# Kernel optimization log

Measured on AMD Instinct MI355X. Metric: run time of the kernel, lower is better.

The kernel has to match this reference:

```python
import jax, jax.numpy as jnp
import numpy as np

B, H, W, C, NH, WS = 8, 113, 113, 512, 8, 7


def setup_inputs() -> dict:
    key = jax.random.key(0)
    k1, k2, k3 = jax.random.split(key, 3)
    x = jax.random.normal(k1, (B, H * W, C), jnp.float32)
    # torch Linear(embed_dims, 3*embed_dims, bias=False); stored as [C, 3C] for x @ W
    w_qkv = jax.random.normal(k2, (C, 3 * C), jnp.float32) * 0.02
    w_proj = jax.random.normal(k3, (C, C), jnp.float32) * 0.02
    b_proj = jnp.zeros((C,), jnp.float32)
    return {"x": x, "w_qkv": w_qkv, "w_proj": w_proj, "b_proj": b_proj, "h": H, "w": W}


def reference(x, w_qkv, w_proj, b_proj, h, w):
    b, n, c = x.shape
    ws, nh = WS, NH
    hd = c // nh
    scale = hd ** -0.5
    pad_b = (ws - h % ws) % ws
    pad_r = (ws - w % ws) % ws
    xi = x.reshape(b, h, w, c)
    xi = jnp.pad(xi, ((0, 0), (0, pad_b), (0, pad_r), (0, 0)))
    Hp, Wp = h + pad_b, w + pad_r
    _h, _w = Hp // ws, Wp // ws
    N = ws * ws
    nw = _h * _w

    # padding mask: 1 on padded rows/cols (matches torch fill of last pad_b rows / pad_r cols;
    # when pad==0 torch fills everything with 1 but mask differences are identically 0 either way)
    rows = jnp.arange(Hp)
    cols = jnp.arange(Wp)
    mask = ((rows[:, None] >= Hp - pad_b) | (cols[None, :] >= Wp - pad_r)).astype(x.dtype)
    mask = mask.reshape(_h, ws, _w, ws).transpose(0, 2, 1, 3).reshape(nw, N)
    am = mask[:, None, :] - mask[:, :, None]  # (nw, N, N)
    am = jnp.where(am != 0, jnp.asarray(-1000.0, x.dtype), jnp.asarray(0.0, x.dtype))

    # window partition: (b, _h, _w, ws, ws, c) -> (b, nw, N, c)
    xw = xi.reshape(b, _h, ws, _w, ws, c).transpose(0, 1, 3, 2, 4, 5).reshape(b, nw, N, c)

    qkv = (xw @ w_qkv).reshape(b, nw, N, 3, nh, hd)
    qkv = jnp.moveaxis(qkv, 3, 0)  # (3, b, nw, N, nh, hd)
    q = qkv[0].transpose(0, 1, 3, 2, 4)  # (b, nw, nh, N, hd)
    k = qkv[1].transpose(0, 1, 3, 2, 4)
    v = qkv[2].transpose(0, 1, 3, 2, 4)

    attn = jnp.einsum('bwhnd,bwhmd->bwhnm', q, k) * scale
    attn = attn + am[None, :, None, :, :]
    attn = jax.nn.softmax(attn, axis=-1)
    out = jnp.einsum('bwhnm,bwhmd->bwhnd', attn, v)  # (b, nw, nh, N, hd)

    # window merge back to (b, Hp, Wp, c)
    out = out.transpose(0, 1, 3, 2, 4).reshape(b, _h, _w, ws, ws, c)
    out = out.transpose(0, 1, 3, 2, 4, 5).reshape(b, Hp, Wp, c)
    out = out[:, :h, :w, :].reshape(b, n, c)
    return out @ w_proj + b_proj
```

## Files before the change

kernel.cpp:

```cpp
#include <hip/hip_runtime.h>
#include <hip/hip_fp16.h>
#include <stdint.h>

typedef _Float16 f16;
typedef __attribute__((ext_vector_type(4))) _Float16 f16x4;
typedef __attribute__((ext_vector_type(8))) _Float16 f16x8;
typedef __attribute__((ext_vector_type(4))) float f32x4;

#define DEVI static __device__ __forceinline__

#define C_DIM 512
#define M1    113288
#define M2    102152
#define NWIN  289
#define NTOK  49
#define NHW   18496

DEVI void load_lds16(const f16* g, f16* l) {
  __builtin_amdgcn_global_load_lds((const __attribute__((address_space(1))) void*)g,
                                   (__attribute__((address_space(3))) void*)l,
                                   16, 0, 0);
}

DEVI f32x4 mfma_16x16x32(f16x8 a, f16x8 b, f32x4 c) {
  return __builtin_amdgcn_mfma_f32_16x16x32_f16(a, b, c, 0, 0, 0);
}

__global__ void cvt_x_kernel(const float* __restrict__ x, f16* __restrict__ xh,
                             f16* __restrict__ zp) {
  if (blockIdx.x == 0 && threadIdx.x < 64) {
    ((int4*)zp)[threadIdx.x] = make_int4(0, 0, 0, 0);
  }
  const int n8 = 6537728;
  int i = blockIdx.x * blockDim.x + threadIdx.x;
  for (; i < n8; i += gridDim.x * blockDim.x) {
    const float4* p = (const float4*)(x) + (size_t)i * 2;
    const float4 a = p[0], b = p[1];
    f16x8 o;
    o[0] = (f16)a.x; o[1] = (f16)a.y; o[2] = (f16)a.z; o[3] = (f16)a.w;
    o[4] = (f16)b.x; o[5] = (f16)b.y; o[6] = (f16)b.z; o[7] = (f16)b.w;
    *(f16x8*)(xh + (size_t)i * 8) = o;
  }
}

__global__ void cvt_wT_kernel(const float* __restrict__ w, f16* __restrict__ wt,
                              int K, int N) {
  const int i = blockIdx.x * blockDim.x + threadIdx.x;
  if (i < K * N) {
    const int n = i / K;
    const int k = i - n * K;
    wt[i] = (f16)w[(size_t)k * N + n];
  }
}

template<int MODE>
__global__ __launch_bounds__(256, 2)
void gemm_kernel(const f16* __restrict__ A, const f16* __restrict__ Bt,
                 f16* __restrict__ qo, f16* __restrict__ ko, f16* __restrict__ vo,
                 float* __restrict__ out, const float* __restrict__ bias,
                 const f16* __restrict__ zp)
{
  __shared__ __align__(16) f16 As[4096];
  __shared__ __align__(16) f16 Bs[4096];

  const int tid  = threadIdx.x;
  const int wave = tid >> 6;
  const int lane = tid & 63;
  const int l16  = lane & 15;
  const int lg   = lane >> 4;

  constexpr int NTN = (MODE == 0) ? 12 : 4;
  const int nwg = gridDim.x;
  const int qq = nwg >> 3, rr = nwg & 7;
  const int xcd = blockIdx.x & 7, ib = blockIdx.x >> 3;
  const int wg = (xcd < rr ? xcd * (qq + 1) : rr * (qq + 1) + (xcd - rr) * qq) + ib;
  const int tn = wg % NTN;
  const int tm = wg / NTN;

  const int srow  = tid >> 2;
  const int chunk = tid & 3;
  const f16* ag[2];
  const f16* bg[2];
  #pragma unroll
  for (int c = 0; c < 2; ++c) {
    const int r  = srow + 64 * c;
    const int lc = chunk ^ ((r >> 1) & 3);
    const int m  = tm * 128 + r;
    long src = 0; bool valid;
    if (MODE == 0) {
      const int b   = m / 14161;
      const int rem = m - b * 14161;
      const int wi  = rem / 49;
      const int t   = rem - wi * 49;
      const int wh = wi / 17, ww = wi - (wi / 17) * 17;
      const int th = t / 7,   tw = t - (t / 7) * 7;
      const int h = wh * 7 + th, w = ww * 7 + tw;
      valid = (m < M1) && (h < 113) && (w < 113);
      src = (long)b * 12769 + h * 113 + w;
    } else {
      const int b = m / 12769;
      const int p = m - b * 12769;
      const int h = p / 113, w = p - (p / 113) * 113;
      valid = (m < M2);
      src = (long)((b * NWIN + (h / 7) * 17 + (w / 7)) * NTOK + (h % 7) * 7 + (w % 7));
    }
    ag[c] = valid ? (A + src * C_DIM + lc * 8) : zp;
    const int rn = tn * 128 + r;
    bg[c] = Bt + (long)rn * C_DIM + lc * 8;
  }
  const f16* a0 = ag[0]; const f16* a1 = ag[1];
  const f16* b0 = bg[0]; const f16* b1 = bg[1];

  int aoff[4], boff[4];
  #pragma unroll
  for (int i = 0; i < 4; ++i) {
    const int ra = (wave >> 1) * 64 + i * 16 + l16;
    aoff[i] = ra * 64 + ((lg ^ ((ra >> 1) & 3)) * 16);
    const int rb = (wave & 1) * 64 + i * 16 + l16;
    boff[i] = rb * 64 + ((lg ^ ((rb >> 1) & 3)) * 16);
  }

  f32x4 acc[4][4];
  #pragma unroll
  for (int i = 0; i < 4; ++i)
    #pragma unroll
    for (int j = 0; j < 4; ++j)
      acc[i][j] = (f32x4){0.f, 0.f, 0.f, 0.f};

  f16* As_w0 = As + wave * 512;
  f16* As_w1 = As + 2048 + wave * 512;
  f16* Bs_w0 = Bs + wave * 512;
  f16* Bs_w1 = Bs + 2048 + wave * 512;

  for (int kk = 0; kk < 16; ++kk) {
    __syncthreads();
    load_lds16(a0, As_w0);
    load_lds16(a1, As_w1);
    load_lds16(b0, Bs_w0);
    load_lds16(b1, Bs_w1);
    a0 += 32; a1 += 32; b0 += 32; b1 += 32;
    __syncthreads();

    f16x8 af[4], bf4[4];
    #pragma unroll
    for (int i = 0; i < 4; ++i) af[i]  = *(const f16x8*)((const char*)As + aoff[i]);
    #pragma unroll
    for (int i = 0; i < 4; ++i) bf4[i] = *(const f16x8*)((const char*)Bs + boff[i]);
    #pragma unroll
    for (int i = 0; i < 4; ++i)
      #pragma unroll
      for (int j = 0; j < 4; ++j)
        acc[i][j] = mfma_16x16x32(af[i], bf4[j], acc[i][j]);
  }

  const int rowb = tm * 128 + (wave >> 1) * 64 + lg * 4;
  const int colb = tn * 128 + (wave & 1) * 64 + l16;
  if (MODE == 0) {
    f16* outw = (tn < 4) ? qo : (tn < 8) ? ko : vo;
    const size_t stride = (tn < 8) ? 3136 : 4096;
    #pragma unroll
    for (int i = 0; i < 4; ++i) {
      #pragma unroll
      for (int j = 0; j < 4; ++j) {
        const int col  = colb + j * 16;
        const int head = (col >> 6) & 7;
        const int d    = col & 63;
        #pragma unroll
        for (int rg = 0; rg < 4; ++rg) {
          const int m = rowb + i * 16 + rg;
          if (m < M1) {
            const int bwi = m / 49;
            const int t   = m - bwi * 49;
            const size_t hw = (size_t)(bwi * 8 + head);
            outw[hw * stride + t * 64 + d] = (f16)acc[i][j][rg];
          }
        }
      }
    }
  } else {
    #pragma unroll
    for (int i = 0; i < 4; ++i) {
      #pragma unroll
      for (int j = 0; j < 4; ++j) {
        const int col = colb + j * 16;
        const float bb = bias[col];
        #pragma unroll
        for (int rg = 0; rg < 4; ++rg) {
          const int m = rowb + i * 16 + rg;
          if (m < M2) out[(size_t)m * C_DIM + col] = acc[i][j][rg] + bb;
        }
      }
    }
  }
}

__global__ __launch_bounds__(256)
void attn_kernel(const f16* __restrict__ qg, const f16* __restrict__ kg,
                 const f16* __restrict__ vg, f16* __restrict__ og)
{
  __shared__ __align__(16) f16 plds[4][4096];
  __shared__ __align__(16) f16 vlds[4][2048];
  const int tid  = threadIdx.x;
  const int wv   = tid >> 6;
  const int lane = tid & 63;
  const int g    = lane >> 4;
  const int c    = lane & 15;
  const int hw   = blockIdx.x * 4 + wv;
  const int bwi  = hw >> 3;
  const int head = hw & 7;
  const int wi   = bwi % NWIN;
  const size_t bqk = (size_t)hw * 3136;
  const f16* vp = vg + (size_t)hw * 4096;

  f16x8 vreg[8];
  #pragma unroll
  for (int d0 = 0; d0 < 8; ++d0)
    vreg[d0] = *(const f16x8*)(vp + lane * 64 + d0 * 8);
  if (lane >= 49) {
    #pragma unroll
    for (int d0 = 0; d0 < 8; ++d0) vreg[d0] = (f16x8){};
  }

  const int wh = wi / 17, ww = wi - (wi / 17) * 17;
  unsigned long long pm = 0;
  if (wh == 16) pm |= (((1ull << 49) - 1) & ~0x7Full);
  if (ww == 16) {
    unsigned long long cm = 0;
    #pragma unroll
    for (int r7 = 0; r7 < 7; ++r7) cm |= 0x7Eull << (7 * r7);
    pm |= cm;
  }

  f32x4 acc[4][4];
  #pragma unroll
  for (int i = 0; i < 4; ++i)
    #pragma unroll
    for (int j = 0; j < 4; ++j) acc[i][j] = (f32x4){0.f, 0.f, 0.f, 0.f};

  const f16* kp = kg + bqk;
  const f16* qp = qg + bqk;
  #pragma unroll
  for (int s = 0; s < 2; ++s) {
    f16x8 kf[4], qf[4];
    #pragma unroll
    for (int i = 0; i < 4; ++i) kf[i] = *(const f16x8*)(kp + (16 * i + c) * 64 + 32 * s + 8 * g);
    #pragma unroll
    for (int j = 0; j < 4; ++j) qf[j] = *(const f16x8*)(qp + (16 * j + c) * 64 + 32 * s + 8 * g);
    #pragma unroll
    for (int i = 0; i < 4; ++i)
      #pragma unroll
      for (int j = 0; j < 4; ++j)
        acc[i][j] = mfma_16x16x32(kf[i], qf[j], acc[i][j]);
  }

  float invs[4];
  #pragma unroll
  for (int j = 0; j < 4; ++j) {
    const int q = 16 * j + c;
    const int padq = (int)((pm >> q) & 1);
    float sj = 0.f;
    #pragma unroll
    for (int i = 0; i < 4; ++i) {
      #pragma unroll
      for (int r = 0; r < 4; ++r) {
        const int key = 16 * i + 4 * g + r;
        const int padk = (int)((pm >> key) & 1);
        float sv = acc[i][j][r] * 0.125f + ((padk ^ padq) ? -1000.f : 0.f);
        float p = __expf(sv);
        if (i == 3) p = ((4 * g + r) == 0) ? p : 0.f;
        acc[i][j][r] = p;
        sj += p;
      }
    }
    invs[j] = sj;
  }
  #pragma unroll
  for (int j = 0; j < 4; ++j) {
    float sj = invs[j];
    sj += __shfl_xor(sj, 16);
    sj += __shfl_xor(sj, 32);
    invs[j] = 1.0f / sj;
  }

  f16* pl = &plds[wv][0];
  const int swz = (c & 7) << 4;
  #pragma unroll
  for (int j = 0; j < 4; ++j) {
    const int q = 16 * j + c;
    const float inv = invs[j];
    #pragma unroll
    for (int i = 0; i < 4; ++i) {
      f16x4 pk;
      pk[0] = (f16)(acc[i][j][0] * inv);
      pk[1] = (f16)(acc[i][j][1] * inv);
      pk[2] = (f16)(acc[i][j][2] * inv);
      pk[3] = (f16)(acc[i][j][3] * inv);
      *(f16x4*)((char*)pl + q * 128 + ((32 * i + 8 * g) ^ swz)) = pk;
    }
  }

  f16* vl = &vlds[wv][0];
  f32x4 o[4][4];
  #pragma unroll
  for (int i = 0; i < 4; ++i)
    #pragma unroll
    for (int j = 0; j < 4; ++j) o[i][j] = (f32x4){0.f, 0.f, 0.f, 0.f};

  #pragma unroll
  for (int h = 0; h < 2; ++h) {
    #pragma unroll
    for (int q4 = 0; q4 < 4; ++q4) {
      const int d0 = 4 * h + q4;
      #pragma unroll
      for (int j = 0; j < 8; ++j) {
        const int dr = (8 * d0 + j) & 31;
        *(f16*)((char*)vl + dr * 128 + ((lane * 2) ^ (j << 4))) = vreg[d0][j];
      }
    }
    #pragma unroll
    for (int s = 0; s < 2; ++s) {
      f16x8 vf[2], pf[4];
      #pragma unroll
      for (int n = 0; n < 2; ++n)
        vf[n] = *(const f16x8*)((const char*)vl + (16 * n + c) * 128 + ((64 * s + 16 * g) ^ swz));
      #pragma unroll
      for (int jq = 0; jq < 4; ++jq)
        pf[jq] = *(const f16x8*)((const char*)pl + (16 * jq + c) * 128 + ((64 * s + 16 * g) ^ swz));
      #pragma unroll
      for (int jq = 0; jq < 4; ++jq)
        #pragma unroll
        for (int n = 0; n < 2; ++n)
          o[jq][2 * h + n] = mfma_16x16x32(pf[jq], vf[n], o[jq][2 * h + n]);
    }
  }

  f16* ob = og + ((size_t)bwi * 49) * 512 + head * 64;
  #pragma unroll
  for (int jq = 0; jq < 4; ++jq) {
    #pragma unroll
    for (int r = 0; r < 4; ++r) {
      const int q = 16 * jq + 4 * g + r;
      if (q < 49) {
        #pragma unroll
        for (int n = 0; n < 4; ++n)
          ob[(size_t)q * 512 + 16 * n + c] = (f16)o[jq][n][r];
      }
    }
  }
}

extern "C" void kernel_launch(void* const* d_in, const int* in_sizes, int n_in,
                              void* d_out, int out_size, void* d_ws, size_t ws_size,
                              hipStream_t stream)
{
  const float* x     = (const float*)d_in[0];
  const float* wqkv  = (const float*)d_in[1];
  const float* wproj = (const float*)d_in[2];
  const float* bproj = (const float*)d_in[3];
  float* out = (float*)d_out;

  char* ws = (char*)d_ws;
  f16* zp = (f16*)ws;
  f16* xh = (f16*)(ws + 1024);
  f16* ah = xh;
  f16* qh = (f16*)(ws + 1024 + 116006912LL);
  f16* kh = qh + 58003456LL;
  f16* vh = kh + 58003456LL;
  f16* wqkvT  = vh + 75759616LL;
  f16* wprojT = wqkvT + 786432LL;

  cvt_x_kernel<<<2048, 256, 0, stream>>>(x, xh, zp);
  cvt_wT_kernel<<<(1536 * 512 + 255) / 256, 256, 0, stream>>>(wqkv, wqkvT, 512, 1536);
  cvt_wT_kernel<<<(512 * 512 + 255) / 256, 256, 0, stream>>>(wproj, wprojT, 512, 512);

  gemm_kernel<0><<<886 * 12, 256, 0, stream>>>(xh, wqkvT, qh, kh, vh, nullptr, nullptr, zp);

  attn_kernel<<<NHW / 4, 256, 0, stream>>>(qh, kh, vh, ah);

  gemm_kernel<1><<<799 * 4, 256, 0, stream>>>(ah, wprojT, nullptr, nullptr, nullptr, out, bproj, zp);
}
```

Before: 580.0 us.

## Rewrite GEMM as 256x256 tile, 8-wave, double-buffered LDS pipeline

Both projection GEMMs now use 512-thread workgroups computing 256x256 output tiles with a K-step of 64. Global-to-LDS loads for the next K block are issued into a second buffer while MFMAs run on the current one, and the loop is split into four phases per K step with explicit waitcnt, barriers and setprio. This aims to hide memory latency and raise data reuse per LDS load. In exchange it uses 128KB of LDS and more accumulator registers per wave, which lowers occupancy, and larger tiles mean more wasted work at the ragged M edge.

```diff
diff --git a/kernel.cpp b/kernel.cpp
--- a/kernel.cpp
+++ b/kernel.cpp
@@ -54,22 +54,24 @@
 }
 
 template<int MODE>
-__global__ __launch_bounds__(256, 2)
+__global__ __launch_bounds__(512, 2)
 void gemm_kernel(const f16* __restrict__ A, const f16* __restrict__ Bt,
                  f16* __restrict__ qo, f16* __restrict__ ko, f16* __restrict__ vo,
                  float* __restrict__ out, const float* __restrict__ bias,
                  const f16* __restrict__ zp)
 {
-  __shared__ __align__(16) f16 As[4096];
-  __shared__ __align__(16) f16 Bs[4096];
+  __shared__ __align__(16) f16 Aq[8][4096];
+  __shared__ __align__(16) f16 Bq[8][4096];
 
   const int tid  = threadIdx.x;
   const int wave = tid >> 6;
   const int lane = tid & 63;
   const int l16  = lane & 15;
-  const int lg   = lane >> 4;
-
-  constexpr int NTN = (MODE == 0) ? 12 : 4;
+  const int g    = lane >> 4;
+  const int wm   = wave >> 2;
+  const int wn   = wave & 3;
+
+  constexpr int NTN = (MODE == 0) ? 6 : 2;
   const int nwg = gridDim.x;
   const int qq = nwg >> 3, rr = nwg & 7;
   const int xcd = blockIdx.x & 7, ib = blockIdx.x >> 3;
@@ -77,15 +79,14 @@
   const int tn = wg % NTN;
   const int tm = wg / NTN;
 
-  const int srow  = tid >> 2;
-  const int chunk = tid & 3;
-  const f16* ag[2];
-  const f16* bg[2];
-  #pragma unroll
-  for (int c = 0; c < 2; ++c) {
-    const int r  = srow + 64 * c;
-    const int lc = chunk ^ ((r >> 1) & 3);
-    const int m  = tm * 128 + r;
+  const int srow  = tid >> 3;
+  const int chunk = tid & 7;
+  const int lc    = chunk ^ (srow & 7);
+  const f16* asrc[4];
+  const f16* bsrc[4];
+  #pragma unroll
+  for (int q = 0; q < 4; ++q) {
+    const int m = tm * 256 + q * 64 + srow;
     long src = 0; bool valid;
     if (MODE == 0) {
       const int b   = m / 14161;
@@ -104,90 +105,138 @@
       valid = (m < M2);
       src = (long)((b * NWIN + (h / 7) * 17 + (w / 7)) * NTOK + (h % 7) * 7 + (w % 7));
     }
-    ag[c] = valid ? (A + src * C_DIM + lc * 8) : zp;
-    const int rn = tn * 128 + r;
-    bg[c] = Bt + (long)rn * C_DIM + lc * 8;
-  }
-  const f16* a0 = ag[0]; const f16* a1 = ag[1];
-  const f16* b0 = bg[0]; const f16* b1 = bg[1];
+    asrc[q] = valid ? (A + src * C_DIM + lc * 8) : zp;
+    bsrc[q] = Bt + (long)(tn * 256 + q * 64 + srow) * C_DIM + lc * 8;
+  }
 
   int aoff[4], boff[4];
   #pragma unroll
   for (int i = 0; i < 4; ++i) {
-    const int ra = (wave >> 1) * 64 + i * 16 + l16;
-    aoff[i] = ra * 64 + ((lg ^ ((ra >> 1) & 3)) * 16);
-    const int rb = (wave & 1) * 64 + i * 16 + l16;
-    boff[i] = rb * 64 + ((lg ^ ((rb >> 1) & 3)) * 16);
-  }
-
-  f32x4 acc[4][4];
-  #pragma unroll
-  for (int i = 0; i < 4; ++i)
+    const int ra = 16 * i + l16;
+    aoff[i] = ra * 128 + ((g ^ (l16 & 7)) * 16);
+    boff[i] = aoff[i];
+  }
+
+  f32x4 acc[8][4];
+  #pragma unroll
+  for (int i = 0; i < 8; ++i)
     #pragma unroll
     for (int j = 0; j < 4; ++j)
       acc[i][j] = (f32x4){0.f, 0.f, 0.f, 0.f};
 
-  f16* As_w0 = As + wave * 512;
-  f16* As_w1 = As + 2048 + wave * 512;
-  f16* Bs_w0 = Bs + wave * 512;
-  f16* Bs_w1 = Bs + 2048 + wave * 512;
-
-  for (int kk = 0; kk < 16; ++kk) {
-    __syncthreads();
-    load_lds16(a0, As_w0);
-    load_lds16(a1, As_w1);
-    load_lds16(b0, Bs_w0);
-    load_lds16(b1, Bs_w1);
-    a0 += 32; a1 += 32; b0 += 32; b1 += 32;
-    __syncthreads();
-
-    f16x8 af[4], bf4[4];
-    #pragma unroll
-    for (int i = 0; i < 4; ++i) af[i]  = *(const f16x8*)((const char*)As + aoff[i]);
-    #pragma unroll
-    for (int i = 0; i < 4; ++i) bf4[i] = *(const f16x8*)((const char*)Bs + boff[i]);
-    #pragma unroll
-    for (int i = 0; i < 4; ++i)
-      #pragma unroll
-      for (int j = 0; j < 4; ++j)
-        acc[i][j] = mfma_16x16x32(af[i], bf4[j], acc[i][j]);
-  }
-
-  const int rowb = tm * 128 + (wave >> 1) * 64 + lg * 4;
-  const int colb = tn * 128 + (wave & 1) * 64 + l16;
+  const int wofs = wave * 512;
+  const char* AqBase = (const char*)&Aq[0][0];
+  const char* BqBase = (const char*)&Bq[0][0];
+
+  load_lds16(asrc[0], &Aq[0][wofs]);
+  load_lds16(asrc[2], &Aq[2][wofs]);
+  load_lds16(bsrc[0], &Bq[0][wofs]);
+  load_lds16(bsrc[1], &Bq[1][wofs]);
+  load_lds16(bsrc[2], &Bq[2][wofs]);
+  load_lds16(bsrc[3], &Bq[3][wofs]);
+  load_lds16(asrc[1], &Aq[1][wofs]);
+  load_lds16(asrc[3], &Aq[3][wofs]);
+  #pragma unroll
+  for (int q = 0; q < 4; ++q) { asrc[q] += 64; bsrc[q] += 64; }
+  asm volatile("s_waitcnt vmcnt(2)" ::: "memory");
+  __builtin_amdgcn_s_barrier();
+
+#define PHASE(MH, KH, STAGE_CODE, TAIL_CODE)                                    \
+  do {                                                                          \
+    const char* Ab = AqBase + (size_t)((PA + 2 * wm + (MH)) * 8192);            \
+    const char* Bb = BqBase + (size_t)((PA + wn) * 8192);                       \
+    f16x8 af[4], bf[4];                                                         \
+    _Pragma("unroll")                                                           \
+    for (int i = 0; i < 4; ++i) af[i] = *(const f16x8*)(Ab + (aoff[i] ^ ((KH) * 64))); \
+    _Pragma("unroll")                                                           \
+    for (int j = 0; j < 4; ++j) bf[j] = *(const f16x8*)(Bb + (boff[j] ^ ((KH) * 64))); \
+    STAGE_CODE;                                                                 \
+    __builtin_amdgcn_s_barrier();                                               \
+    asm volatile("s_waitcnt lgkmcnt(0)" ::: "memory");                          \
+    __builtin_amdgcn_sched_barrier(0);                                          \
+    __builtin_amdgcn_s_setprio(1);                                              \
+    _Pragma("unroll")                                                           \
+    for (int i = 0; i < 4; ++i)                                                 \
+      _Pragma("unroll")                                                         \
+      for (int j = 0; j < 4; ++j)                                               \
+        acc[(MH) * 4 + i][j] = mfma_16x16x32(af[i], bf[j], acc[(MH) * 4 + i][j]); \
+    __builtin_amdgcn_s_setprio(0);                                              \
+    TAIL_CODE;                                                                  \
+    __builtin_amdgcn_s_barrier();                                               \
+  } while (0)
+
+  for (int t = 0; t < 7; ++t) {
+    const int PA  = (t & 1) * 4;
+    const int PB1 = 4 - PA;
+    PHASE(0, 0,
+      { load_lds16(asrc[0], &Aq[PB1 + 0][wofs]);
+        load_lds16(asrc[2], &Aq[PB1 + 2][wofs]); },
+      {});
+    PHASE(0, 1,
+      { load_lds16(bsrc[0], &Bq[PB1 + 0][wofs]);
+        load_lds16(bsrc[1], &Bq[PB1 + 1][wofs]);
+        load_lds16(bsrc[2], &Bq[PB1 + 2][wofs]);
+        load_lds16(bsrc[3], &Bq[PB1 + 3][wofs]); },
+      { asm volatile("s_waitcnt vmcnt(6)" ::: "memory"); });
+    PHASE(1, 0, {}, {});
+    PHASE(1, 1,
+      { load_lds16(asrc[1], &Aq[PB1 + 1][wofs]);
+        load_lds16(asrc[3], &Aq[PB1 + 3][wofs]);
+        _Pragma("unroll")
+        for (int q = 0; q < 4; ++q) { asrc[q] += 64; bsrc[q] += 64; } },
+      { asm volatile("s_waitcnt vmcnt(2)" ::: "memory"); });
+  }
+  {
+    const int PA = 4;
+    PHASE(0, 0, {}, {});
+    PHASE(0, 1, {}, { asm volatile("s_waitcnt vmcnt(0)" ::: "memory"); });
+    PHASE(1, 0, {}, {});
+    PHASE(1, 1, {}, {});
+  }
+#undef PHASE
+
+  const int rowb = tm * 256 + wm * 128 + g * 4;
+  const int colb = tn * 256 + wn * 64 + l16;
   if (MODE == 0) {
-    f16* outw = (tn < 4) ? qo : (tn < 8) ? ko : vo;
-    const size_t stride = (tn < 8) ? 3136 : 4096;
-    #pragma unroll
-    for (int i = 0; i < 4; ++i) {
-      #pragma unroll
-      for (int j = 0; j < 4; ++j) {
-        const int col  = colb + j * 16;
-        const int head = (col >> 6) & 7;
-        const int d    = col & 63;
+    const int cwi  = tn * 4 + wn;
+    f16* outw = (cwi < 8) ? qo : (cwi < 16) ? ko : vo;
+    const size_t stride = (cwi < 16) ? 3136 : 4096;
+    const int head = cwi & 7;
+    #pragma unroll
+    for (int mh = 0; mh < 2; ++mh) {
+      #pragma unroll
+      for (int i = 0; i < 4; ++i) {
         #pragma unroll
         for (int rg = 0; rg < 4; ++rg) {
-          const int m = rowb + i * 16 + rg;
+          const int m = rowb + mh * 64 + i * 16 + rg;
           if (m < M1) {
             const int bwi = m / 49;
             const int t   = m - bwi * 49;
-            const size_t hw = (size_t)(bwi * 8 + head);
-            outw[hw * stride + t * 64 + d] = (f16)acc[i][j][rg];
+            f16* orow = outw + (size_t)(bwi * 8 + head) * stride + t * 64 + l16;
+            #pragma unroll
+            for (int j = 0; j < 4; ++j)
+              orow[j * 16] = (f16)acc[mh * 4 + i][j][rg];
           }
         }
       }
     }
   } else {
-    #pragma unroll
-    for (int i = 0; i < 4; ++i) {
-      #pragma unroll
-      for (int j = 0; j < 4; ++j) {
-        const int col = colb + j * 16;
-        const float bb = bias[col];
+    float bb[4];
+    #pragma unroll
+    for (int j = 0; j < 4; ++j) bb[j] = bias[colb + j * 16];
+    #pragma unroll
+    for (int mh = 0; mh < 2; ++mh) {
+      #pragma unroll
+      for (int i = 0; i < 4; ++i) {
         #pragma unroll
         for (int rg = 0; rg < 4; ++rg) {
-          const int m = rowb + i * 16 + rg;
-          if (m < M2) out[(size_t)m * C_DIM + col] = acc[i][j][rg] + bb;
+          const int m = rowb + mh * 64 + i * 16 + rg;
+          if (m < M2) {
+            float* orow = out + (size_t)m * C_DIM + colb;
+            #pragma unroll
+            for (int j = 0; j < 4; ++j)
+              orow[j * 16] = acc[mh * 4 + i][j][rg] + bb[j];
+          }
         }
       }
     }
@@ -373,9 +422,9 @@
   cvt_wT_kernel<<<(1536 * 512 + 255) / 256, 256, 0, stream>>>(wqkv, wqkvT, 512, 1536);
   cvt_wT_kernel<<<(512 * 512 + 255) / 256, 256, 0, stream>>>(wproj, wprojT, 512, 512);
 
-  gemm_kernel<0><<<886 * 12, 256, 0, stream>>>(xh, wqkvT, qh, kh, vh, nullptr, nullptr, zp);
+  gemm_kernel<0><<<443 * 6, 512, 0, stream>>>(xh, wqkvT, qh, kh, vh, nullptr, nullptr, zp);
 
   attn_kernel<<<NHW / 4, 256, 0, stream>>>(qh, kh, vh, ah);
 
-  gemm_kernel<1><<<799 * 4, 256, 0, stream>>>(ah, wprojT, nullptr, nullptr, nullptr, out, bproj, zp);
-}
+  gemm_kernel<1><<<400 * 2, 512, 0, stream>>>(ah, wprojT, nullptr, nullptr, nullptr, out, bproj, zp);
+}
```

After: 567.9 us. 1.02x faster.
